# Performance work log

Hardware: AMD Instinct MI355X
Metric: run time of the kernel (lower is better)

The kernel has to match this reference:

```python
import jax, jax.numpy as jnp
import numpy as np

TOP_N = 16  # min(top_n=16, num_cmp_blocks=256)


def setup_inputs() -> dict:
    key = jax.random.key(0)
    k1, k2, k3, k4 = jax.random.split(key, 4)
    B, H, N, D = 4, 16, 4096, 64
    M = 256  # num_cmp_blocks
    return {
        "q": jax.random.normal(k1, (B, H, N, D), dtype=jnp.float32),
        "compressed_k": jax.random.normal(k2, (B, H, M, D), dtype=jnp.float32),
        "k": jax.random.normal(k3, (B, H, N, D), dtype=jnp.float32),
        "v": jax.random.normal(k4, (B, H, N, D), dtype=jnp.float32),
    }


def reference(q, compressed_k, k, v):
    # q: (B,H,N,D), compressed_k: (B,H,M,D)
    D = q.shape[-1]
    scale = D ** -0.5
    # scaled QK^T against compressed keys -> (B,H,N,M), stable softmax over M
    scores = jnp.einsum("bhnd,bhmd->bhnm", q, compressed_k) * scale
    compressed_scores = jax.nn.softmax(scores, axis=-1)
    # cross-head importance reduction -> (B,N,M)
    importance = compressed_scores.sum(axis=1)
    _, top_indices = jax.lax.top_k(importance, TOP_N)  # (B,N,TOP_N)
    return (top_indices, compressed_scores)
```

## Files before the change

### kernel.cpp

```cpp
#include <hip/hip_runtime.h>
#include <math.h>

#define BB   4
#define HH   16
#define NN   4096
#define DD   64
#define MM   256
#define TOPN 16
#define ROWS 32
#define NTILES (NN / ROWS)

__global__ __launch_bounds__(256)
void k_scores(const float* __restrict__ q, const float* __restrict__ ck,
              float* __restrict__ out_scores, float* __restrict__ imp_out,
              int hpb) {
  __shared__ float ckT[DD][MM / 2];
  __shared__ float qT[DD][ROWS];

  const int bx  = blockIdx.x;
  const int hg  = blockIdx.y;
  const int b   = bx / NTILES;
  const int n0  = (bx % NTILES) * ROWS;
  const int tid = threadIdx.x;
  const int rg  = tid >> 5;
  const int c   = tid & 31;

  float imp[4][8];
#pragma unroll
  for (int i = 0; i < 4; i++)
#pragma unroll
    for (int k = 0; k < 8; k++) imp[i][k] = 0.0f;

  const int h_end = (hg + 1) * hpb;
  for (int h = hg * hpb; h < h_end; ++h) {
    float acc[4][8];
#pragma unroll
    for (int i = 0; i < 4; i++)
#pragma unroll
      for (int k = 0; k < 8; k++) acc[i][k] = 0.0f;

#pragma unroll
    for (int hh = 0; hh < 2; ++hh) {
      __syncthreads();

      if (hh == 0) {
        const int row = tid & 31;
        const int dch = tid >> 5;
        const float* qp =
            q + (((size_t)(b * HH + h) * NN) + n0 + row) * DD + dch * 8;
        const float4 a0 = *(const float4*)(qp);
        const float4 a1 = *(const float4*)(qp + 4);
        const float s = 0.125f;
        qT[dch * 8 + 0][row] = a0.x * s;
        qT[dch * 8 + 1][row] = a0.y * s;
        qT[dch * 8 + 2][row] = a0.z * s;
        qT[dch * 8 + 3][row] = a0.w * s;
        qT[dch * 8 + 4][row] = a1.x * s;
        qT[dch * 8 + 5][row] = a1.y * s;
        qT[dch * 8 + 6][row] = a1.z * s;
        qT[dch * 8 + 7][row] = a1.w * s;
      }
      {
        const int mrow = tid & 127;
        const int dh   = tid >> 7;
        const float* cp =
            ck + (((size_t)(b * HH + h) * MM) + hh * 128 + mrow) * DD + dh * 32;
#pragma unroll
        for (int k = 0; k < 8; k++) {
          const float4 a = *(const float4*)(cp + k * 4);
          ckT[dh * 32 + k * 4 + 0][mrow] = a.x;
          ckT[dh * 32 + k * 4 + 1][mrow] = a.y;
          ckT[dh * 32 + k * 4 + 2][mrow] = a.z;
          ckT[dh * 32 + k * 4 + 3][mrow] = a.w;
        }
      }
      __syncthreads();

#pragma unroll 8
      for (int d = 0; d < DD; ++d) {
        const float4 qv = *(const float4*)&qT[d][rg * 4];
        const float2 c0 = *(const float2*)&ckT[d][2 * c];
        const float2 c1 = *(const float2*)&ckT[d][64 + 2 * c];
        const float qa0 = qv.x, qa1 = qv.y, qa2 = qv.z, qa3 = qv.w;
        acc[0][hh * 4 + 0] = fmaf(qa0, c0.x, acc[0][hh * 4 + 0]);
        acc[0][hh * 4 + 1] = fmaf(qa0, c0.y, acc[0][hh * 4 + 1]);
        acc[0][hh * 4 + 2] = fmaf(qa0, c1.x, acc[0][hh * 4 + 2]);
        acc[0][hh * 4 + 3] = fmaf(qa0, c1.y, acc[0][hh * 4 + 3]);
        acc[1][hh * 4 + 0] = fmaf(qa1, c0.x, acc[1][hh * 4 + 0]);
        acc[1][hh * 4 + 1] = fmaf(qa1, c0.y, acc[1][hh * 4 + 1]);
        acc[1][hh * 4 + 2] = fmaf(qa1, c1.x, acc[1][hh * 4 + 2]);
        acc[1][hh * 4 + 3] = fmaf(qa1, c1.y, acc[1][hh * 4 + 3]);
        acc[2][hh * 4 + 0] = fmaf(qa2, c0.x, acc[2][hh * 4 + 0]);
        acc[2][hh * 4 + 1] = fmaf(qa2, c0.y, acc[2][hh * 4 + 1]);
        acc[2][hh * 4 + 2] = fmaf(qa2, c1.x, acc[2][hh * 4 + 2]);
        acc[2][hh * 4 + 3] = fmaf(qa2, c1.y, acc[2][hh * 4 + 3]);
        acc[3][hh * 4 + 0] = fmaf(qa3, c0.x, acc[3][hh * 4 + 0]);
        acc[3][hh * 4 + 1] = fmaf(qa3, c0.y, acc[3][hh * 4 + 1]);
        acc[3][hh * 4 + 2] = fmaf(qa3, c1.x, acc[3][hh * 4 + 2]);
        acc[3][hh * 4 + 3] = fmaf(qa3, c1.y, acc[3][hh * 4 + 3]);
      }
    }

#pragma unroll
    for (int i = 0; i < 4; i++) {
      float mx = acc[i][0];
#pragma unroll
      for (int k = 1; k < 8; k++) mx = fmaxf(mx, acc[i][k]);
#pragma unroll
      for (int off = 1; off < 32; off <<= 1)
        mx = fmaxf(mx, __shfl_xor(mx, off, 64));

      float sum = 0.0f;
#pragma unroll
      for (int k = 0; k < 8; k++) {
        acc[i][k] = __expf(acc[i][k] - mx);
        sum += acc[i][k];
      }
#pragma unroll
      for (int off = 1; off < 32; off <<= 1) sum += __shfl_xor(sum, off, 64);

      const float inv = 1.0f / sum;
#pragma unroll
      for (int k = 0; k < 8; k++) acc[i][k] *= inv;

      float* op =
          out_scores + (((size_t)(b * HH + h) * NN) + n0 + rg * 4 + i) * MM;
      *(float2*)(op + 2 * c)       = make_float2(acc[i][0], acc[i][1]);
      *(float2*)(op + 64 + 2 * c)  = make_float2(acc[i][2], acc[i][3]);
      *(float2*)(op + 128 + 2 * c) = make_float2(acc[i][4], acc[i][5]);
      *(float2*)(op + 192 + 2 * c) = make_float2(acc[i][6], acc[i][7]);

#pragma unroll
      for (int k = 0; k < 8; k++) imp[i][k] += acc[i][k];
    }
  }

  if (imp_out != nullptr) {
    float* base = imp_out + (size_t)hg * BB * NN * MM;
#pragma unroll
    for (int i = 0; i < 4; i++) {
      float* op = base + ((size_t)b * NN + n0 + rg * 4 + i) * MM;
      *(float2*)(op + 2 * c)       = make_float2(imp[i][0], imp[i][1]);
      *(float2*)(op + 64 + 2 * c)  = make_float2(imp[i][2], imp[i][3]);
      *(float2*)(op + 128 + 2 * c) = make_float2(imp[i][4], imp[i][5]);
      *(float2*)(op + 192 + 2 * c) = make_float2(imp[i][6], imp[i][7]);
    }
  }
}

__device__ __forceinline__ void topk_row(float vals[4], int lane, int b, int n,
                                         float* __restrict__ out_idx) {
  int keep = 0;
#pragma unroll
  for (int it = 0; it < TOPN; ++it) {
    float bv = vals[0];
    int bi = lane * 4;
#pragma unroll
    for (int j = 1; j < 4; j++) {
      if (vals[j] > bv) { bv = vals[j]; bi = lane * 4 + j; }
    }
    for (int off = 1; off < 64; off <<= 1) {
      const float ov = __shfl_xor(bv, off, 64);
      const int oi = __shfl_xor(bi, off, 64);
      if (ov > bv || (ov == bv && oi < bi)) { bv = ov; bi = oi; }
    }
    if (lane == it) keep = bi;
    if ((bi >> 2) == lane) vals[bi & 3] = -INFINITY;
  }
  if (lane < TOPN)
    out_idx[((size_t)b * NN + n) * TOPN + lane] = (float)keep;
}

__global__ __launch_bounds__(256)
void k_topk(const float* __restrict__ imp, float* __restrict__ out_idx,
            int nsplit) {
  const int wave = blockIdx.x * 4 + (threadIdx.x >> 6);
  const int lane = threadIdx.x & 63;
  const int b = wave >> 12;
  const int n = wave & (NN - 1);
  float vals[4] = {0.f, 0.f, 0.f, 0.f};
  for (int s = 0; s < nsplit; ++s) {
    const float4 v = *(const float4*)(imp + (size_t)s * BB * NN * MM +
                                      ((size_t)b * NN + n) * MM + lane * 4);
    vals[0] += v.x; vals[1] += v.y; vals[2] += v.z; vals[3] += v.w;
  }
  topk_row(vals, lane, b, n, out_idx);
}

__global__ __launch_bounds__(256)
void k_topk_from_scores(const float* __restrict__ scores,
                        float* __restrict__ out_idx) {
  const int wave = blockIdx.x * 4 + (threadIdx.x >> 6);
  const int lane = threadIdx.x & 63;
  const int b = wave >> 12;
  const int n = wave & (NN - 1);
  float vals[4] = {0.f, 0.f, 0.f, 0.f};
  for (int h = 0; h < HH; ++h) {
    const float4 s = *(const float4*)(scores +
                                      (((size_t)(b * HH + h) * NN) + n) * MM +
                                      lane * 4);
    vals[0] += s.x; vals[1] += s.y; vals[2] += s.z; vals[3] += s.w;
  }
  topk_row(vals, lane, b, n, out_idx);
}

extern "C" void kernel_launch(void* const* d_in, const int* in_sizes, int n_in,
                              void* d_out, int out_size, void* d_ws,
                              size_t ws_size, hipStream_t stream) {
  const float* q  = (const float*)d_in[0];
  const float* ck = (const float*)d_in[1];

  float* out        = (float*)d_out;
  float* out_idx    = out;
  float* out_scores = out + (size_t)BB * NN * TOPN;

  const size_t one = (size_t)BB * NN * MM * sizeof(float);

  int hsplit;
  float* imp;
  if (ws_size >= 2 * one) { hsplit = 2; imp = (float*)d_ws; }
  else if (ws_size >= one) { hsplit = 1; imp = (float*)d_ws; }
  else { hsplit = 1; imp = nullptr; }

  dim3 grid(BB * NTILES, hsplit);
  k_scores<<<grid, 256, 0, stream>>>(q, ck, out_scores, imp, HH / hsplit);

  if (imp != nullptr) {
    k_topk<<<(BB * NN) / 4, 256, 0, stream>>>(imp, out_idx, hsplit);
  } else {
    k_topk_from_scores<<<(BB * NN) / 4, 256, 0, stream>>>(out_scores, out_idx);
  }
}
```

Measured before the change: 211.8 us.

## Retile score GEMM to 8 rows x 4 contiguous columns per thread with float4 stores

```diff
diff --git a/kernel.cpp b/kernel.cpp
--- a/kernel.cpp
+++ b/kernel.cpp
@@ -14,40 +14,52 @@
 void k_scores(const float* __restrict__ q, const float* __restrict__ ck,
               float* __restrict__ out_scores, float* __restrict__ imp_out,
               int hpb) {
-  __shared__ float ckT[DD][MM / 2];
+  __shared__ float ckT[32][MM];
   __shared__ float qT[DD][ROWS];
 
-  const int bx  = blockIdx.x;
-  const int hg  = blockIdx.y;
-  const int b   = bx / NTILES;
-  const int n0  = (bx % NTILES) * ROWS;
-  const int tid = threadIdx.x;
-  const int rg  = tid >> 5;
-  const int c   = tid & 31;
-
-  float imp[4][8];
-#pragma unroll
-  for (int i = 0; i < 4; i++)
-#pragma unroll
-    for (int k = 0; k < 8; k++) imp[i][k] = 0.0f;
+  const int bx   = blockIdx.x;
+  const int hg   = blockIdx.y;
+  const int b    = bx / NTILES;
+  const int n0   = (bx % NTILES) * ROWS;
+  const int tid  = threadIdx.x;
+  const int lane = tid & 63;
+  const int r0   = (tid >> 6) * 8;
+
+  float imp[8][4];
+#pragma unroll
+  for (int i = 0; i < 8; i++)
+#pragma unroll
+    for (int j = 0; j < 4; j++) imp[i][j] = 0.0f;
 
   const int h_end = (hg + 1) * hpb;
   for (int h = hg * hpb; h < h_end; ++h) {
-    float acc[4][8];
-#pragma unroll
-    for (int i = 0; i < 4; i++)
-#pragma unroll
-      for (int k = 0; k < 8; k++) acc[i][k] = 0.0f;
-
-#pragma unroll
-    for (int hh = 0; hh < 2; ++hh) {
+    float acc[8][4];
+#pragma unroll
+    for (int i = 0; i < 8; i++)
+#pragma unroll
+      for (int j = 0; j < 4; j++) acc[i][j] = 0.0f;
+
+#pragma unroll
+    for (int kc = 0; kc < 2; ++kc) {
       __syncthreads();
 
-      if (hh == 0) {
+      {
+        const float* cp =
+            ck + ((size_t)(b * HH + h) * MM + tid) * DD + kc * 32;
+#pragma unroll
+        for (int j = 0; j < 8; ++j) {
+          const float4 a = *(const float4*)(cp + j * 4);
+          ckT[j * 4 + 0][tid] = a.x;
+          ckT[j * 4 + 1][tid] = a.y;
+          ckT[j * 4 + 2][tid] = a.z;
+          ckT[j * 4 + 3][tid] = a.w;
+        }
+      }
+      if (kc == 0) {
         const int row = tid & 31;
         const int dch = tid >> 5;
         const float* qp =
-            q + (((size_t)(b * HH + h) * NN) + n0 + row) * DD + dch * 8;
+            q + ((size_t)(b * HH + h) * NN + n0 + row) * DD + dch * 8;
         const float4 a0 = *(const float4*)(qp);
         const float4 a1 = *(const float4*)(qp + 4);
         const float s = 0.125f;
@@ -60,90 +72,85 @@
         qT[dch * 8 + 6][row] = a1.z * s;
         qT[dch * 8 + 7][row] = a1.w * s;
       }
-      {
-        const int mrow = tid & 127;
-        const int dh   = tid >> 7;
-        const float* cp =
-            ck + (((size_t)(b * HH + h) * MM) + hh * 128 + mrow) * DD + dh * 32;
-#pragma unroll
-        for (int k = 0; k < 8; k++) {
-          const float4 a = *(const float4*)(cp + k * 4);
-          ckT[dh * 32 + k * 4 + 0][mrow] = a.x;
-          ckT[dh * 32 + k * 4 + 1][mrow] = a.y;
-          ckT[dh * 32 + k * 4 + 2][mrow] = a.z;
-          ckT[dh * 32 + k * 4 + 3][mrow] = a.w;
-        }
-      }
       __syncthreads();
 
 #pragma unroll 8
-      for (int d = 0; d < DD; ++d) {
-        const float4 qv = *(const float4*)&qT[d][rg * 4];
-        const float2 c0 = *(const float2*)&ckT[d][2 * c];
-        const float2 c1 = *(const float2*)&ckT[d][64 + 2 * c];
-        const float qa0 = qv.x, qa1 = qv.y, qa2 = qv.z, qa3 = qv.w;
-        acc[0][hh * 4 + 0] = fmaf(qa0, c0.x, acc[0][hh * 4 + 0]);
-        acc[0][hh * 4 + 1] = fmaf(qa0, c0.y, acc[0][hh * 4 + 1]);
-        acc[0][hh * 4 + 2] = fmaf(qa0, c1.x, acc[0][hh * 4 + 2]);
-        acc[0][hh * 4 + 3] = fmaf(qa0, c1.y, acc[0][hh * 4 + 3]);
-        acc[1][hh * 4 + 0] = fmaf(qa1, c0.x, acc[1][hh * 4 + 0]);
-        acc[1][hh * 4 + 1] = fmaf(qa1, c0.y, acc[1][hh * 4 + 1]);
-        acc[1][hh * 4 + 2] = fmaf(qa1, c1.x, acc[1][hh * 4 + 2]);
-        acc[1][hh * 4 + 3] = fmaf(qa1, c1.y, acc[1][hh * 4 + 3]);
-        acc[2][hh * 4 + 0] = fmaf(qa2, c0.x, acc[2][hh * 4 + 0]);
-        acc[2][hh * 4 + 1] = fmaf(qa2, c0.y, acc[2][hh * 4 + 1]);
-        acc[2][hh * 4 + 2] = fmaf(qa2, c1.x, acc[2][hh * 4 + 2]);
-        acc[2][hh * 4 + 3] = fmaf(qa2, c1.y, acc[2][hh * 4 + 3]);
-        acc[3][hh * 4 + 0] = fmaf(qa3, c0.x, acc[3][hh * 4 + 0]);
-        acc[3][hh * 4 + 1] = fmaf(qa3, c0.y, acc[3][hh * 4 + 1]);
-        acc[3][hh * 4 + 2] = fmaf(qa3, c1.x, acc[3][hh * 4 + 2]);
-        acc[3][hh * 4 + 3] = fmaf(qa3, c1.y, acc[3][hh * 4 + 3]);
-      }
-    }
-
-#pragma unroll
-    for (int i = 0; i < 4; i++) {
-      float mx = acc[i][0];
-#pragma unroll
-      for (int k = 1; k < 8; k++) mx = fmaxf(mx, acc[i][k]);
-#pragma unroll
-      for (int off = 1; off < 32; off <<= 1)
+      for (int dd = 0; dd < 32; ++dd) {
+        const float4 cv = *(const float4*)&ckT[dd][lane * 4];
+        const float4 q0 = *(const float4*)&qT[kc * 32 + dd][r0];
+        const float4 q1 = *(const float4*)&qT[kc * 32 + dd][r0 + 4];
+        acc[0][0] = fmaf(q0.x, cv.x, acc[0][0]);
+        acc[0][1] = fmaf(q0.x, cv.y, acc[0][1]);
+        acc[0][2] = fmaf(q0.x, cv.z, acc[0][2]);
+        acc[0][3] = fmaf(q0.x, cv.w, acc[0][3]);
+        acc[1][0] = fmaf(q0.y, cv.x, acc[1][0]);
+        acc[1][1] = fmaf(q0.y, cv.y, acc[1][1]);
+        acc[1][2] = fmaf(q0.y, cv.z, acc[1][2]);
+        acc[1][3] = fmaf(q0.y, cv.w, acc[1][3]);
+        acc[2][0] = fmaf(q0.z, cv.x, acc[2][0]);
+        acc[2][1] = fmaf(q0.z, cv.y, acc[2][1]);
+        acc[2][2] = fmaf(q0.z, cv.z, acc[2][2]);
+        acc[2][3] = fmaf(q0.z, cv.w, acc[2][3]);
+        acc[3][0] = fmaf(q0.w, cv.x, acc[3][0]);
+        acc[3][1] = fmaf(q0.w, cv.y, acc[3][1]);
+        acc[3][2] = fmaf(q0.w, cv.z, acc[3][2]);
+        acc[3][3] = fmaf(q0.w, cv.w, acc[3][3]);
+        acc[4][0] = fmaf(q1.x, cv.x, acc[4][0]);
+        acc[4][1] = fmaf(q1.x, cv.y, acc[4][1]);
+        acc[4][2] = fmaf(q1.x, cv.z, acc[4][2]);
+        acc[4][3] = fmaf(q1.x, cv.w, acc[4][3]);
+        acc[5][0] = fmaf(q1.y, cv.x, acc[5][0]);
+        acc[5][1] = fmaf(q1.y, cv.y, acc[5][1]);
+        acc[5][2] = fmaf(q1.y, cv.z, acc[5][2]);
+        acc[5][3] = fmaf(q1.y, cv.w, acc[5][3]);
+        acc[6][0] = fmaf(q1.z, cv.x, acc[6][0]);
+        acc[6][1] = fmaf(q1.z, cv.y, acc[6][1]);
+        acc[6][2] = fmaf(q1.z, cv.z, acc[6][2]);
+        acc[6][3] = fmaf(q1.z, cv.w, acc[6][3]);
+        acc[7][0] = fmaf(q1.w, cv.x, acc[7][0]);
+        acc[7][1] = fmaf(q1.w, cv.y, acc[7][1]);
+        acc[7][2] = fmaf(q1.w, cv.z, acc[7][2]);
+        acc[7][3] = fmaf(q1.w, cv.w, acc[7][3]);
+      }
+    }
+
+#pragma unroll
+    for (int i = 0; i < 8; i++) {
+      float mx = fmaxf(fmaxf(acc[i][0], acc[i][1]), fmaxf(acc[i][2], acc[i][3]));
+#pragma unroll
+      for (int off = 1; off < 64; off <<= 1)
         mx = fmaxf(mx, __shfl_xor(mx, off, 64));
 
       float sum = 0.0f;
 #pragma unroll
-      for (int k = 0; k < 8; k++) {
-        acc[i][k] = __expf(acc[i][k] - mx);
-        sum += acc[i][k];
-      }
-#pragma unroll
-      for (int off = 1; off < 32; off <<= 1) sum += __shfl_xor(sum, off, 64);
+      for (int j = 0; j < 4; j++) {
+        acc[i][j] = __expf(acc[i][j] - mx);
+        sum += acc[i][j];
+      }
+#pragma unroll
+      for (int off = 1; off < 64; off <<= 1) sum += __shfl_xor(sum, off, 64);
 
       const float inv = 1.0f / sum;
 #pragma unroll
-      for (int k = 0; k < 8; k++) acc[i][k] *= inv;
+      for (int j = 0; j < 4; j++) {
+        acc[i][j] *= inv;
+        imp[i][j] += acc[i][j];
+      }
 
       float* op =
-          out_scores + (((size_t)(b * HH + h) * NN) + n0 + rg * 4 + i) * MM;
-      *(float2*)(op + 2 * c)       = make_float2(acc[i][0], acc[i][1]);
-      *(float2*)(op + 64 + 2 * c)  = make_float2(acc[i][2], acc[i][3]);
-      *(float2*)(op + 128 + 2 * c) = make_float2(acc[i][4], acc[i][5]);
-      *(float2*)(op + 192 + 2 * c) = make_float2(acc[i][6], acc[i][7]);
-
-#pragma unroll
-      for (int k = 0; k < 8; k++) imp[i][k] += acc[i][k];
+          out_scores + ((size_t)(b * HH + h) * NN + n0 + r0 + i) * MM;
+      *(float4*)(op + lane * 4) =
+          make_float4(acc[i][0], acc[i][1], acc[i][2], acc[i][3]);
     }
   }
 
   if (imp_out != nullptr) {
     float* base = imp_out + (size_t)hg * BB * NN * MM;
 #pragma unroll
-    for (int i = 0; i < 4; i++) {
-      float* op = base + ((size_t)b * NN + n0 + rg * 4 + i) * MM;
-      *(float2*)(op + 2 * c)       = make_float2(imp[i][0], imp[i][1]);
-      *(float2*)(op + 64 + 2 * c)  = make_float2(imp[i][2], imp[i][3]);
-      *(float2*)(op + 128 + 2 * c) = make_float2(imp[i][4], imp[i][5]);
-      *(float2*)(op + 192 + 2 * c) = make_float2(imp[i][6], imp[i][7]);
+    for (int i = 0; i < 8; i++) {
+      float* op = base + ((size_t)b * NN + n0 + r0 + i) * MM;
+      *(float4*)(op + lane * 4) =
+          make_float4(imp[i][0], imp[i][1], imp[i][2], imp[i][3]);
     }
   }
 }
```

Measured after the change: 236.3 us. 1.12x slower.
